# Optimization experiments

Hardware: AMD Instinct MI355X
Metric: run time of the kernel (lower is better)

## Reference

```python
import jax, jax.numpy as jnp
import numpy as np

N_MESH, N_GRID, N_EDGE = 2562, 16384, 49152
D, EDGE_DIM, OUT_DIM = 512, 4, 128
LN_EPS = 1e-5


def _mlp_ln(x, w1, b1, w2, b2, g, beta):
    # Linear -> ReLU -> Linear -> LayerNorm (activate_final=False, use_layer_norm=True)
    h = jax.nn.relu(x @ w1 + b1)
    h = h @ w2 + b2
    mu = jnp.mean(h, axis=-1, keepdims=True)
    var = jnp.var(h, axis=-1, keepdims=True)
    return (h - mu) * jax.lax.rsqrt(var + LN_EPS) * g + beta


def setup_inputs() -> dict:
    key = jax.random.key(0)
    ks = iter(jax.random.split(key, 40))

    def W(i, o):
        return (jax.random.normal(next(ks), (i, o), jnp.float32) / np.float32(np.sqrt(i)))

    inp = {
        "input_mesh_nodes": jax.random.normal(next(ks), (N_MESH, D), jnp.float32),
        "input_grid_nodes": jax.random.normal(next(ks), (N_GRID, D), jnp.float32),
        "input_edge_attr": jax.random.normal(next(ks), (N_EDGE, EDGE_DIM), jnp.float32),
        "edge_index": jnp.stack([
            jax.random.randint(next(ks), (N_EDGE,), 0, N_MESH, jnp.int32),  # senders (mesh)
            jax.random.randint(next(ks), (N_EDGE,), 0, N_GRID, jnp.int32),  # receivers (grid)
        ], axis=0),
        # edges_mlp: EDGE_DIM -> D -> D, LN
        "emlp_w1": W(EDGE_DIM, D), "emlp_b1": jnp.zeros((D,), jnp.float32),
        "emlp_w2": W(D, D), "emlp_b2": jnp.zeros((D,), jnp.float32),
        "emlp_g": jnp.ones((D,), jnp.float32), "emlp_beta": jnp.zeros((D,), jnp.float32),
        # gnn message MLP: 3D -> D -> D, LN   (cat(x_i, x_j, edge_attr))
        "ge_w1": W(3 * D, D), "ge_b1": jnp.zeros((D,), jnp.float32),
        "ge_w2": W(D, D), "ge_b2": jnp.zeros((D,), jnp.float32),
        "ge_g": jnp.ones((D,), jnp.float32), "ge_beta": jnp.zeros((D,), jnp.float32),
        # gnn node MLP: 2D -> D -> D, LN   (cat(receiver_x, aggr))
        "gn_w1": W(2 * D, D), "gn_b1": jnp.zeros((D,), jnp.float32),
        "gn_w2": W(D, D), "gn_b2": jnp.zeros((D,), jnp.float32),
        "gn_g": jnp.ones((D,), jnp.float32), "gn_beta": jnp.zeros((D,), jnp.float32),
        # grid_mlp_final: D -> D -> OUT_DIM, LN
        "fin_w1": W(D, D), "fin_b1": jnp.zeros((D,), jnp.float32),
        "fin_w2": W(D, OUT_DIM), "fin_b2": jnp.zeros((OUT_DIM,), jnp.float32),
        "fin_g": jnp.ones((OUT_DIM,), jnp.float32), "fin_beta": jnp.zeros((OUT_DIM,), jnp.float32),
    }
    return inp


def reference(input_mesh_nodes, input_grid_nodes, input_edge_attr, edge_index,
              emlp_w1, emlp_b1, emlp_w2, emlp_b2, emlp_g, emlp_beta,
              ge_w1, ge_b1, ge_w2, ge_b2, ge_g, ge_beta,
              gn_w1, gn_b1, gn_w2, gn_b2, gn_g, gn_beta,
              fin_w1, fin_b1, fin_w2, fin_b2, fin_g, fin_beta):
    # edge embedding MLP
    edges_emb = _mlp_ln(input_edge_attr, emlp_w1, emlp_b1, emlp_w2, emlp_b2, emlp_g, emlp_beta)
    senders, receivers = edge_index[0], edge_index[1]
    x_i = input_grid_nodes[receivers]   # receiver (grid) features gathered per edge
    x_j = input_mesh_nodes[senders]     # sender (mesh) features gathered per edge
    # per-edge message MLP on cat(x_i, x_j, edge_attr)
    msg = _mlp_ln(jnp.concatenate([x_i, x_j, edges_emb], axis=-1),
                  ge_w1, ge_b1, ge_w2, ge_b2, ge_g, ge_beta)  # [E, D]
    # scatter-add messages to receiver grid nodes (aggr='add')
    aggr = jax.ops.segment_sum(msg, receivers, num_segments=N_GRID)  # [N_GRID, D]
    # node update MLP on cat(receiver_x, aggr)
    gnn_out = _mlp_ln(jnp.concatenate([input_grid_nodes, aggr], axis=-1),
                      gn_w1, gn_b1, gn_w2, gn_b2, gn_g, gn_beta)
    latent_grid_nodes = input_grid_nodes + gnn_out  # residual
    return _mlp_ln(latent_grid_nodes, fin_w1, fin_b1, fin_w2, fin_b2, fin_g, fin_beta)
```

## Files before the change

### kernel.cpp

```cpp
#include <hip/hip_runtime.h>
#include <hip/hip_bf16.h>
#include <stdint.h>

#define LN_EPS 1e-5f

typedef __hip_bfloat16 bf16;
typedef short short8 __attribute__((ext_vector_type(8)));
typedef float f32x4 __attribute__((ext_vector_type(4)));

static __device__ __forceinline__ float bf2f(short s) {
    unsigned int u = ((unsigned int)(unsigned short)s) << 16;
    return __uint_as_float(u);
}
static __device__ __forceinline__ short f2bf(float x) {
    __hip_bfloat16 h = __float2bfloat16(x);
    return *reinterpret_cast<short*>(&h);
}

static __device__ __forceinline__ void gload16(const void* g, void* l) {
    __builtin_amdgcn_global_load_lds((const __attribute__((address_space(1))) void*)g,
                                     (__attribute__((address_space(3))) void*)l, 16, 0, 0);
}

struct TDesc { const float* src; bf16* dst; int K; int N; int kOff; const float* scale; };
struct TDescs { TDesc d[9]; };

__global__ void transpose_all_kernel(TDescs descs) {
    TDesc t = descs.d[blockIdx.z];
    int kb = blockIdx.x * 32, nb = blockIdx.y * 32;
    if (kb >= t.K || nb >= t.N) return;
    __shared__ float tile[32][33];
    int tx = threadIdx.x & 31, ty = threadIdx.x >> 5;
    for (int i = ty; i < 32; i += 8) {
        int k = kb + i, n = nb + tx;
        float v = (k < t.K && n < t.N) ? t.src[(size_t)(t.kOff + k) * t.N + n] : 0.f;
        if (t.scale && k < t.K) v *= t.scale[k];
        tile[i][tx] = v;
    }
    __syncthreads();
    for (int i = ty; i < 32; i += 8) {
        int n = nb + i, k = kb + tx;
        if (n < t.N && k < t.K)
            t.dst[(size_t)n * t.K + k] = __float2bfloat16(tile[tx][i]);
    }
}

__global__ void uv_kernel(const float* __restrict__ W, const float* __restrict__ g,
                          const float* __restrict__ be, float* __restrict__ u,
                          float* __restrict__ v) {
    int n = blockIdx.x * 256 + threadIdx.x;
    if (n >= 512) return;
    float su = 0.f, sv = 0.f;
    for (int k = 0; k < 512; k++) {
        float w = W[(size_t)(1024 + k) * 512 + n];
        su += g[k] * w;
        sv += be[k] * w;
    }
    u[n] = su;
    v[n] = sv;
}

__global__ void cvt_bf16_kernel(const float* __restrict__ src, bf16* __restrict__ dst, int n) {
    int i = blockIdx.x * 256 + threadIdx.x;
    int idx = i * 4;
    if (idx >= n) return;
    float4 v = *(const float4*)(src + idx);
    dst[idx + 0] = __float2bfloat16(v.x);
    dst[idx + 1] = __float2bfloat16(v.y);
    dst[idx + 2] = __float2bfloat16(v.z);
    dst[idx + 3] = __float2bfloat16(v.w);
}

__global__ void edge_l1_kernel(const float* __restrict__ attr, const float* __restrict__ w1,
                               const float* __restrict__ b1, bf16* __restrict__ h1, int E) {
    int e = blockIdx.x * 4 + (threadIdx.x >> 6);
    if (e >= E) return;
    int lane = threadIdx.x & 63;
    int d0 = lane * 8;
    float4 a = *(const float4*)(attr + (size_t)e * 4);
    float av[4] = {a.x, a.y, a.z, a.w};
    float s[8];
    {
        float4 c0 = *(const float4*)(b1 + d0), c1 = *(const float4*)(b1 + d0 + 4);
        s[0]=c0.x; s[1]=c0.y; s[2]=c0.z; s[3]=c0.w; s[4]=c1.x; s[5]=c1.y; s[6]=c1.z; s[7]=c1.w;
    }
#pragma unroll
    for (int k = 0; k < 4; k++) {
        float4 w0 = *(const float4*)(w1 + k * 512 + d0);
        float4 w1v = *(const float4*)(w1 + k * 512 + d0 + 4);
        float wv[8] = {w0.x, w0.y, w0.z, w0.w, w1v.x, w1v.y, w1v.z, w1v.w};
#pragma unroll
        for (int j = 0; j < 8; j++) s[j] += av[k] * wv[j];
    }
    short8 o;
#pragma unroll
    for (int j = 0; j < 8; j++) o[j] = f2bf(fmaxf(s[j], 0.f));
    *(short8*)(h1 + (size_t)e * 512 + d0) = o;
}

template <int EPI>
__global__ __launch_bounds__(256, 2) void gemm_bt_kernel(
    const bf16* __restrict__ A, const bf16* __restrict__ BT,
    const float* __restrict__ bias, bf16* __restrict__ C, int M, int N, int K,
    const bf16* __restrict__ gridp, const bf16* __restrict__ meshp,
    const int* __restrict__ send, const int* __restrict__ recv,
    const float2* __restrict__ stats, const float* __restrict__ uvec,
    const float* __restrict__ vvec, float* __restrict__ OutF) {
    __shared__ short SMEM[2 * 2 * 128 * 64];
    const int t = threadIdx.x;
    const int lane = t & 63, w = t >> 6;
    const int wm = w >> 1, wn = w & 1;
    const int lr = lane & 15, lh = lane >> 4;

    int gx = gridDim.x;
    int nwg = gx * gridDim.y;
    int orig = blockIdx.y * gx + blockIdx.x;
    int q = nwg >> 3, r = nwg & 7;
    int xcd = orig & 7, loc = orig >> 3;
    int wg = (xcd < r ? xcd * (q + 1) : r * (q + 1) + (xcd - r) * q) + loc;
    int bx = wg % gx, by = wg / gx;
    const int row0 = by * 128;
    const int col0 = bx * 128;

    const int sr3 = lane >> 3;
    const int su = (lane & 7) ^ sr3;
    const int srow = w * 32 + sr3;
    const int scol = su * 8;
    const bf16* gaP[4];
    const bf16* gbP[4];
#pragma unroll
    for (int i = 0; i < 4; i++) {
        int ra = row0 + srow + i * 8; if (ra >= M) ra = M - 1;
        int rb = col0 + srow + i * 8; if (rb >= N) rb = N - 1;
        gaP[i] = A + (size_t)ra * K + scol;
        gbP[i] = BT + (size_t)rb * K + scol;
    }

    auto STAGE = [&](int b, int k0) {
        short* la = SMEM + b * 16384 + w * 32 * 64;
        short* lb = la + 8192;
#pragma unroll
        for (int i = 0; i < 4; i++) {
            gload16(gaP[i] + k0, la + i * 8 * 64);
            gload16(gbP[i] + k0, lb + i * 8 * 64);
        }
    };

    f32x4 acc[4][4];
#pragma unroll
    for (int i = 0; i < 4; i++)
#pragma unroll
        for (int j = 0; j < 4; j++) acc[i][j] = {0.f, 0.f, 0.f, 0.f};

    const int T = K >> 6;
    STAGE(0, 0);

    int cur = 0;
    for (int tt = 0; tt < T; ++tt) {
        if (tt + 1 < T) {
            STAGE(cur ^ 1, (tt + 1) << 6);
            asm volatile("s_waitcnt vmcnt(8)" ::: "memory");
        } else {
            asm volatile("s_waitcnt vmcnt(0)" ::: "memory");
        }
        __builtin_amdgcn_s_barrier();
        asm volatile("" ::: "memory");

        const short* Ac = SMEM + cur * 16384;
        const short* Bc = Ac + 8192;
#pragma unroll
        for (int kk = 0; kk < 64; kk += 32) {
            short8 af[4], bfv[4];
#pragma unroll
            for (int mf = 0; mf < 4; mf++) {
                int rowa = wm * 64 + mf * 16 + lr;
                int ua = ((kk >> 3) + lh) ^ (rowa & 7);
                af[mf] = *(const short8*)&Ac[rowa * 64 + ua * 8];
            }
#pragma unroll
            for (int nf = 0; nf < 4; nf++) {
                int rowb = wn * 64 + nf * 16 + lr;
                int ub = ((kk >> 3) + lh) ^ (rowb & 7);
                bfv[nf] = *(const short8*)&Bc[rowb * 64 + ub * 8];
            }
#pragma unroll
            for (int mf = 0; mf < 4; mf++)
#pragma unroll
                for (int nf = 0; nf < 4; nf++)
                    acc[mf][nf] = __builtin_amdgcn_mfma_f32_16x16x32_bf16(
                        af[mf], bfv[nf], acc[mf][nf], 0, 0, 0);
        }
        asm volatile("" ::: "memory");
        __builtin_amdgcn_s_barrier();
        cur ^= 1;
    }

    if (EPI == 5) {
        short* Cs = SMEM;
#pragma unroll
        for (int nf = 0; nf < 4; nf++) {
            float bv = bias[wn * 64 + nf * 16 + lr];
#pragma unroll
            for (int mf = 0; mf < 4; mf++)
#pragma unroll
                for (int r2 = 0; r2 < 4; r2++) {
                    int rl = wm * 64 + mf * 16 + lh * 4 + r2;
                    Cs[rl * 132 + wn * 64 + nf * 16 + lr] = f2bf(acc[mf][nf][r2] + bv);
                }
        }
        __syncthreads();
        int rl = w * 32 + (lane >> 1);
        int half = lane & 1;
        short8 vs[8];
        float s = 0.f, s2 = 0.f;
#pragma unroll
        for (int j8 = 0; j8 < 8; j8++) {
            vs[j8] = *(const short8*)&Cs[rl * 132 + half * 64 + j8 * 8];
#pragma unroll
            for (int j = 0; j < 8; j++) {
                float f = bf2f(vs[j8][j]);
                s += f; s2 += f * f;
            }
        }
        s += __shfl_xor(s, 1, 64);
        s2 += __shfl_xor(s2, 1, 64);
        float mu = s * (1.f / 128.f);
        float var = s2 * (1.f / 128.f) - mu * mu;
        float rs = rsqrtf(var + LN_EPS);
        int grow = row0 + rl;
#pragma unroll
        for (int j8 = 0; j8 < 8; j8++) {
            int c0 = half * 64 + j8 * 8;
            float4 g0 = *(const float4*)(uvec + c0), g1 = *(const float4*)(uvec + c0 + 4);
            float4 b0 = *(const float4*)(vvec + c0), b1v = *(const float4*)(vvec + c0 + 4);
            float gg[8] = {g0.x, g0.y, g0.z, g0.w, g1.x, g1.y, g1.z, g1.w};
            float bb[8] = {b0.x, b0.y, b0.z, b0.w, b1v.x, b1v.y, b1v.z, b1v.w};
            float4 o0, o1;
            float* op = (float*)&o0;
#pragma unroll
            for (int j = 0; j < 8; j++) {
                float y = (bf2f(vs[j8][j]) - mu) * rs * gg[j] + bb[j];
                if (j < 4) ((float*)&o0)[j] = y; else ((float*)&o1)[j - 4] = y;
            }
            (void)op;
            *(float4*)(OutF + (size_t)grow * 128 + c0) = o0;
            *(float4*)(OutF + (size_t)grow * 128 + c0 + 4) = o1;
        }
        return;
    }

    short* Cw = SMEM + w * (32 * 66);
    const int rgrp = lane >> 3, u = lane & 7;
#pragma unroll
    for (int hp = 0; hp < 2; hp++) {
#pragma unroll
        for (int mf2 = 0; mf2 < 2; mf2++) {
            int mf = hp * 2 + mf2;
#pragma unroll
            for (int nf = 0; nf < 4; nf++)
#pragma unroll
                for (int r2 = 0; r2 < 4; r2++) {
                    int rl = mf2 * 16 + lh * 4 + r2;
                    Cw[rl * 66 + nf * 16 + lr] = f2bf(acc[mf][nf][r2]);
                }
        }
#pragma unroll
        for (int rr = 0; rr < 4; rr++) {
            int rl = rr * 8 + rgrp;
            int grow = row0 + wm * 64 + hp * 32 + rl;
            int gcol = col0 + wn * 64 + u * 8;
            short8 vv = *(const short8*)&Cw[rl * 66 + u * 8];
            float vf[8];
#pragma unroll
            for (int j = 0; j < 8; j++) vf[j] = bf2f(vv[j]);
            if (EPI == 4) {
                int e = grow < M ? grow : M - 1;
                float2 st = stats[e];
                float rs = st.y, mrs = st.x * st.y;
                float4 u0 = *(const float4*)(uvec + gcol), u1 = *(const float4*)(uvec + gcol + 4);
                float4 v0 = *(const float4*)(vvec + gcol), v1 = *(const float4*)(vvec + gcol + 4);
                float uu[8] = {u0.x, u0.y, u0.z, u0.w, u1.x, u1.y, u1.z, u1.w};
                float vvv[8] = {v0.x, v0.y, v0.z, v0.w, v1.x, v1.y, v1.z, v1.w};
#pragma unroll
                for (int j = 0; j < 8; j++) vf[j] = rs * vf[j] - mrs * uu[j] + vvv[j];
            }
            if (EPI >= 1) {
                float4 c0 = *(const float4*)(bias + gcol);
                float4 c1 = *(const float4*)(bias + gcol + 4);
                float bb[8] = {c0.x, c0.y, c0.z, c0.w, c1.x, c1.y, c1.z, c1.w};
#pragma unroll
                for (int j = 0; j < 8; j++) vf[j] += bb[j];
            }
            if (EPI == 4) {
                int e = grow < M ? grow : M - 1;
                int rn = recv[e], sn = send[e];
                short8 gp = *(const short8*)(gridp + (size_t)rn * 512 + gcol);
                short8 mp = *(const short8*)(meshp + (size_t)sn * 512 + gcol);
#pragma unroll
                for (int j = 0; j < 8; j++) vf[j] += bf2f(gp[j]) + bf2f(mp[j]);
            }
            if (EPI == 2 || EPI == 4) {
#pragma unroll
                for (int j = 0; j < 8; j++) vf[j] = fmaxf(vf[j], 0.f);
            }
            short8 o;
#pragma unroll
            for (int j = 0; j < 8; j++) o[j] = f2bf(vf[j]);
            if (grow < M && gcol < N)
                *(short8*)(C + (size_t)grow * N + gcol) = o;
        }
    }
}

__global__ void ln_resid_kernel(const bf16* __restrict__ X, const float* __restrict__ gw,
                                const float* __restrict__ bw, bf16* __restrict__ outb,
                                const bf16* __restrict__ resid, int R) {
    int row = blockIdx.x * 4 + (threadIdx.x >> 6);
    if (row >= R) return;
    int lane = threadIdx.x & 63;
    short8 t8 = *(const short8*)(X + (size_t)row * 512 + lane * 8);
    float v[8];
#pragma unroll
    for (int j = 0; j < 8; j++) v[j] = bf2f(t8[j]);
    float s = 0.f, s2 = 0.f;
#pragma unroll
    for (int j = 0; j < 8; j++) { s += v[j]; s2 += v[j] * v[j]; }
#pragma unroll
    for (int o = 32; o > 0; o >>= 1) {
        s += __shfl_xor(s, o, 64);
        s2 += __shfl_xor(s2, o, 64);
    }
    float mu = s * (1.f / 512.f);
    float var = s2 * (1.f / 512.f) - mu * mu;
    float rs = rsqrtf(var + LN_EPS);
    int d0 = lane * 8;
    short8 rv = *(const short8*)(resid + (size_t)row * 512 + d0);
    short8 o;
#pragma unroll
    for (int j = 0; j < 8; j++) {
        float y = (v[j] - mu) * rs * gw[d0 + j] + bw[d0 + j];
        o[j] = f2bf(bf2f(rv[j]) + y);
    }
    *(short8*)(outb + (size_t)row * 512 + d0) = o;
}

__global__ void ln_stats_kernel(const bf16* __restrict__ X, float2* __restrict__ stats, int R) {
    int row = blockIdx.x * 4 + (threadIdx.x >> 6);
    if (row >= R) return;
    int lane = threadIdx.x & 63;
    short8 t8 = *(const short8*)(X + (size_t)row * 512 + lane * 8);
    float s = 0.f, s2 = 0.f;
#pragma unroll
    for (int j = 0; j < 8; j++) {
        float x = bf2f(t8[j]);
        s += x; s2 += x * x;
    }
#pragma unroll
    for (int o = 32; o > 0; o >>= 1) {
        s += __shfl_xor(s, o, 64);
        s2 += __shfl_xor(s2, o, 64);
    }
    float mu = s * (1.f / 512.f);
    float var = s2 * (1.f / 512.f) - mu * mu;
    if (lane == 0) stats[row] = make_float2(mu, rsqrtf(var + LN_EPS));
}

__global__ void degree_kernel(const int* __restrict__ recv, int* __restrict__ deg, int E) {
    int e = blockIdx.x * 256 + threadIdx.x;
    if (e < E) atomicAdd(&deg[recv[e]], 1);
}

__global__ void scan_kernel(const int* __restrict__ deg, int* __restrict__ off) {
    __shared__ int partial[1024];
    int t = threadIdx.x;
    int base = t * 16;
    int v[16];
    int s = 0;
#pragma unroll
    for (int i = 0; i < 16; i++) { v[i] = deg[base + i]; s += v[i]; }
    partial[t] = s;
    __syncthreads();
    for (int o = 1; o < 1024; o <<= 1) {
        int x = (t >= o) ? partial[t - o] : 0;
        __syncthreads();
        partial[t] += x;
        __syncthreads();
    }
    int run = (t == 0) ? 0 : partial[t - 1];
#pragma unroll
    for (int i = 0; i < 16; i++) { off[base + i] = run; run += v[i]; }
    if (t == 1023) off[16384] = run;
}

__global__ void scatter_kernel(const int* __restrict__ recv, const int* __restrict__ off,
                               int* __restrict__ cnt, int* __restrict__ edges, int E) {
    int e = blockIdx.x * 256 + threadIdx.x;
    if (e < E) {
        int r = recv[e];
        int p = atomicAdd(&cnt[r], 1);
        edges[off[r] + p] = e;
    }
}

__global__ void aggregate_kernel(const bf16* __restrict__ T5, const float2* __restrict__ stats,
                                 const float* __restrict__ gw, const float* __restrict__ bw,
                                 const bf16* __restrict__ gridb,
                                 const int* __restrict__ off, const int* __restrict__ edges,
                                 bf16* __restrict__ X2, int G) {
    int g = blockIdx.x * 4 + (threadIdx.x >> 6);
    if (g >= G) return;
    int lane = threadIdx.x & 63;
    int d0 = lane * 8;
    float gg[8], bb[8];
    {
        float4 a = *(const float4*)(gw + d0), b = *(const float4*)(gw + d0 + 4);
        gg[0]=a.x; gg[1]=a.y; gg[2]=a.z; gg[3]=a.w; gg[4]=b.x; gg[5]=b.y; gg[6]=b.z; gg[7]=b.w;
        float4 c = *(const float4*)(bw + d0), d = *(const float4*)(bw + d0 + 4);
        bb[0]=c.x; bb[1]=c.y; bb[2]=c.z; bb[3]=c.w; bb[4]=d.x; bb[5]=d.y; bb[6]=d.z; bb[7]=d.w;
    }
    float s[8] = {0.f, 0.f, 0.f, 0.f, 0.f, 0.f, 0.f, 0.f};
    int a = off[g], b = off[g + 1];
    for (int i = a; i < b; i++) {
        int e = edges[i];
        float2 st = stats[e];
        short8 m = *(const short8*)(T5 + (size_t)e * 512 + d0);
#pragma unroll
        for (int j = 0; j < 8; j++)
            s[j] += (bf2f(m[j]) - st.x) * st.y * gg[j] + bb[j];
    }
    *(short8*)(X2 + (size_t)g * 1024 + d0) = *(const short8*)(gridb + (size_t)g * 512 + d0);
    short8 o;
#pragma unroll
    for (int j = 0; j < 8; j++) o[j] = f2bf(s[j]);
    *(short8*)(X2 + (size_t)g * 1024 + 512 + d0) = o;
}

extern "C" void kernel_launch(void* const* d_in, const int* in_sizes, int n_in,
                              void* d_out, int out_size, void* d_ws, size_t ws_size,
                              hipStream_t stream) {
    const int NM = 2562, NG = 16384, NE = 49152;
    const float* mesh   = (const float*)d_in[0];
    const float* grid   = (const float*)d_in[1];
    const float* attr   = (const float*)d_in[2];
    const int*   eidx   = (const int*)d_in[3];
    const int*   send   = eidx;
    const int*   recv   = eidx + NE;
    const float* emlp_w1 = (const float*)d_in[4];
    const float* emlp_b1 = (const float*)d_in[5];
    const float* emlp_w2 = (const float*)d_in[6];
    const float* emlp_b2 = (const float*)d_in[7];
    const float* emlp_g  = (const float*)d_in[8];
    const float* emlp_be = (const float*)d_in[9];
    const float* ge_w1 = (const float*)d_in[10];
    const float* ge_b1 = (const float*)d_in[11];
    const float* ge_w2 = (const float*)d_in[12];
    const float* ge_b2 = (const float*)d_in[13];
    const float* ge_g  = (const float*)d_in[14];
    const float* ge_be = (const float*)d_in[15];
    const float* gn_w1 = (const float*)d_in[16];
    const float* gn_b1 = (const float*)d_in[17];
    const float* gn_w2 = (const float*)d_in[18];
    const float* gn_b2 = (const float*)d_in[19];
    const float* gn_g  = (const float*)d_in[20];
    const float* gn_be = (const float*)d_in[21];
    const float* fin_w1 = (const float*)d_in[22];
    const float* fin_b1 = (const float*)d_in[23];
    const float* fin_w2 = (const float*)d_in[24];
    const float* fin_b2 = (const float*)d_in[25];
    const float* fin_g  = (const float*)d_in[26];
    const float* fin_be = (const float*)d_in[27];

    char* p = (char*)d_ws;
    auto take = [&](size_t bytes) -> char* {
        char* r = p;
        p += (bytes + 255) & ~(size_t)255;
        return r;
    };
    bf16* emlp_w2T = (bf16*)take((size_t)512 * 512 * 2);
    bf16* geA_T    = (bf16*)take((size_t)512 * 512 * 2);
    bf16* geB_T    = (bf16*)take((size_t)512 * 512 * 2);
    bf16* geC_T    = (bf16*)take((size_t)512 * 512 * 2);
    bf16* ge_w2T   = (bf16*)take((size_t)512 * 512 * 2);
    bf16* gn_w1T   = (bf16*)take((size_t)512 * 1024 * 2);
    bf16* gn_w2T   = (bf16*)take((size_t)512 * 512 * 2);
    bf16* fin_w1T  = (bf16*)take((size_t)512 * 512 * 2);
    bf16* fin_w2T  = (bf16*)take((size_t)128 * 512 * 2);
    bf16* grid_bf  = (bf16*)take((size_t)NG * 512 * 2);
    bf16* mesh_bf  = (bf16*)take((size_t)NM * 512 * 2);
    bf16* bufA     = (bf16*)take((size_t)NE * 512 * 2);
    bf16* bufB     = (bf16*)take((size_t)NE * 512 * 2);
    bf16* bufC     = (bf16*)take((size_t)NG * 512 * 2);
    bf16* bufD     = (bf16*)take((size_t)NM * 512 * 2);
    float2* stats  = (float2*)take((size_t)NE * 8);
    float* uvecW   = (float*)take((size_t)512 * 4);
    float* vvecW   = (float*)take((size_t)512 * 4);
    int*  deg      = (int*)take((size_t)NG * 4);
    int*  cnt      = (int*)take((size_t)NG * 4);
    int*  csr_off  = (int*)take((size_t)(NG + 1) * 4);
    int*  csr_edge = (int*)take((size_t)NE * 4);

    const bf16* nbf = nullptr; const int* ni = nullptr;
    const float2* nst = nullptr; const float* nf = nullptr; float* nff = nullptr;

    TDescs td;
    td.d[0] = {emlp_w2, emlp_w2T, 512, 512, 0, nullptr};
    td.d[1] = {ge_w1,   geA_T,    512, 512, 0, nullptr};
    td.d[2] = {ge_w1,   geB_T,    512, 512, 512, nullptr};
    td.d[3] = {ge_w1,   geC_T,    512, 512, 1024, emlp_g};
    td.d[4] = {ge_w2,   ge_w2T,   512, 512, 0, nullptr};
    td.d[5] = {gn_w1,   gn_w1T,  1024, 512, 0, nullptr};
    td.d[6] = {gn_w2,   gn_w2T,   512, 512, 0, nullptr};
    td.d[7] = {fin_w1,  fin_w1T,  512, 512, 0, nullptr};
    td.d[8] = {fin_w2,  fin_w2T,  512, 128, 0, nullptr};
    hipLaunchKernelGGL(transpose_all_kernel, dim3(32, 16, 9), dim3(256), 0, stream, td);
    hipLaunchKernelGGL(uv_kernel, dim3(2), dim3(256), 0, stream,
                       ge_w1, emlp_g, emlp_be, uvecW, vvecW);

    hipLaunchKernelGGL(cvt_bf16_kernel, dim3((NG * 512 / 4 + 255) / 256), dim3(256), 0, stream,
                       grid, grid_bf, NG * 512);
    hipLaunchKernelGGL(cvt_bf16_kernel, dim3((NM * 512 / 4 + 255) / 256), dim3(256), 0, stream,
                       mesh, mesh_bf, NM * 512);
    hipMemsetAsync(deg, 0, (size_t)NG * 4, stream);
    hipMemsetAsync(cnt, 0, (size_t)NG * 4, stream);
    hipLaunchKernelGGL(degree_kernel, dim3((NE + 255) / 256), dim3(256), 0, stream, recv, deg, NE);
    hipLaunchKernelGGL(scan_kernel, dim3(1), dim3(1024), 0, stream, deg, csr_off);
    hipLaunchKernelGGL(scatter_kernel, dim3((NE + 255) / 256), dim3(256), 0, stream,
                       recv, csr_off, cnt, csr_edge, NE);

    hipLaunchKernelGGL(edge_l1_kernel, dim3(NE / 4), dim3(256), 0, stream,
                       attr, emlp_w1, emlp_b1, bufA, NE);
    hipLaunchKernelGGL(gemm_bt_kernel<1>, dim3(4, NE / 128), dim3(256), 0, stream,
                       bufA, emlp_w2T, emlp_b2, bufB, NE, 512, 512,
                       nbf, nbf, ni, ni, nst, nf, nf, nff);
    hipLaunchKernelGGL(ln_stats_kernel, dim3(NE / 4), dim3(256), 0, stream, bufB, stats, NE);

    hipLaunchKernelGGL(gemm_bt_kernel<0>, dim3(4, NG / 128), dim3(256), 0, stream,
                       grid_bf, geA_T, nf, bufC, NG, 512, 512,
                       nbf, nbf, ni, ni, nst, nf, nf, nff);
    hipLaunchKernelGGL(gemm_bt_kernel<0>, dim3(4, (NM + 127) / 128), dim3(256), 0, stream,
                       mesh_bf, geB_T, nf, bufD, NM, 512, 512,
                       nbf, nbf, ni, ni, nst, nf, nf, nff);
    hipLaunchKernelGGL(gemm_bt_kernel<4>, dim3(4, NE / 128), dim3(256), 0, stream,
                       bufB, geC_T, ge_b1, bufA, NE, 512, 512,
                       bufC, bufD, send, recv, stats, uvecW, vvecW, nff);
    hipLaunchKernelGGL(gemm_bt_kernel<1>, dim3(4, NE / 128), dim3(256), 0, stream,
                       bufA, ge_w2T, ge_b2, bufB, NE, 512, 512,
                       nbf, nbf, ni, ni, nst, nf, nf, nff);
    hipLaunchKernelGGL(ln_stats_kernel, dim3(NE / 4), dim3(256), 0, stream, bufB, stats, NE);
    hipLaunchKernelGGL(aggregate_kernel, dim3(NG / 4), dim3(256), 0, stream,
                       bufB, stats, ge_g, ge_be, grid_bf, csr_off, csr_edge, bufA, NG);

    hipLaunchKernelGGL(gemm_bt_kernel<2>, dim3(4, NG / 128), dim3(256), 0, stream,
                       bufA, gn_w1T, gn_b1, bufC, NG, 512, 1024,
                       nbf, nbf, ni, ni, nst, nf, nf, nff);
    hipLaunchKernelGGL(gemm_bt_kernel<1>, dim3(4, NG / 128), dim3(256), 0, stream,
                       bufC, gn_w2T, gn_b2, bufB, NG, 512, 512,
                       nbf, nbf, ni, ni, nst, nf, nf, nff);
    hipLaunchKernelGGL(ln_resid_kernel, dim3(NG / 4), dim3(256), 0, stream,
                       bufB, gn_g, gn_be, bufA, grid_bf, NG);

    hipLaunchKernelGGL(gemm_bt_kernel<2>, dim3(4, NG / 128), dim3(256), 0, stream,
                       bufA, fin_w1T, fin_b1, bufC, NG, 512, 512,
                       nbf, nbf, ni, ni, nst, nf, nf, nff);
    hipLaunchKernelGGL(gemm_bt_kernel<5>, dim3(1, NG / 128), dim3(256), 0, stream,
                       bufC, fin_w2T, fin_b2, (bf16*)nullptr, NG, 128, 512,
                       nbf, nbf, ni, ni, nst, fin_g, fin_be, (float*)d_out);
}
```

Measured before the change: 353.2 us.

## Add 8-wave 256x128 GEMM kernel with split-K staging for large GEMMs

Adds a gemm8 kernel that uses 512 threads and a 256x128 output tile. It interleaves the A-tile prefetch with the first half-K MFMA block and the B-tile prefetch with the second half, and raises wave priority around the MFMAs. The large edge and grid GEMMs now use it, while the mesh GEMM and the final LN GEMM keep the old kernel, which is reduced to its EPI 0/5 paths. The goal is to cut B reloads per output and overlap loads with compute, at the cost of one block per CU and fewer workgroups.

```diff
diff --git a/kernel.cpp b/kernel.cpp
--- a/kernel.cpp
+++ b/kernel.cpp
@@ -99,13 +99,206 @@
 }
 
 template <int EPI>
-__global__ __launch_bounds__(256, 2) void gemm_bt_kernel(
+__global__ __launch_bounds__(512, 1) void gemm8_kernel(
     const bf16* __restrict__ A, const bf16* __restrict__ BT,
     const float* __restrict__ bias, bf16* __restrict__ C, int M, int N, int K,
     const bf16* __restrict__ gridp, const bf16* __restrict__ meshp,
     const int* __restrict__ send, const int* __restrict__ recv,
     const float2* __restrict__ stats, const float* __restrict__ uvec,
-    const float* __restrict__ vvec, float* __restrict__ OutF) {
+    const float* __restrict__ vvec) {
+    __shared__ short SMEM[2 * (256 + 128) * 64];
+    const int t = threadIdx.x;
+    const int lane = t & 63, w = t >> 6;
+    const int wm = w >> 1, wn = w & 1;
+    const int lr = lane & 15, lh = lane >> 4;
+
+    int gx = gridDim.x;
+    int nwg = gx * gridDim.y;
+    int orig = blockIdx.y * gx + blockIdx.x;
+    int q = nwg >> 3, r = nwg & 7;
+    int xcd = orig & 7, loc = orig >> 3;
+    int wg = (xcd < r ? xcd * (q + 1) : r * (q + 1) + (xcd - r) * q) + loc;
+    int bx = wg % gx, by = wg / gx;
+    const int row0 = by * 256;
+    const int col0 = bx * 128;
+
+    const int sr3 = lane >> 3;
+    const int su = (lane & 7) ^ sr3;
+    const int scol = su * 8;
+    const bf16* gaP[4];
+    const bf16* gbP[2];
+#pragma unroll
+    for (int c = 0; c < 4; c++) {
+        int ra = row0 + c * 64 + w * 8 + sr3; if (ra >= M) ra = M - 1;
+        gaP[c] = A + (size_t)ra * K + scol;
+    }
+#pragma unroll
+    for (int c = 0; c < 2; c++) {
+        int rb = col0 + c * 64 + w * 8 + sr3; if (rb >= N) rb = N - 1;
+        gbP[c] = BT + (size_t)rb * K + scol;
+    }
+
+    auto STAGE_A = [&](int b, int k0) {
+        short* la = SMEM + b * 24576;
+#pragma unroll
+        for (int c = 0; c < 4; c++)
+            gload16(gaP[c] + k0, la + (c * 64 + w * 8) * 64);
+    };
+    auto STAGE_B = [&](int b, int k0) {
+        short* lb = SMEM + b * 24576 + 16384;
+#pragma unroll
+        for (int c = 0; c < 2; c++)
+            gload16(gbP[c] + k0, lb + (c * 64 + w * 8) * 64);
+    };
+
+    f32x4 acc[4][4];
+#pragma unroll
+    for (int i = 0; i < 4; i++)
+#pragma unroll
+        for (int j = 0; j < 4; j++) acc[i][j] = {0.f, 0.f, 0.f, 0.f};
+
+    const int T = K >> 6;
+    STAGE_A(0, 0);
+    STAGE_B(0, 0);
+
+    for (int tt = 0; tt < T; ++tt) {
+        const int bc = tt & 1;
+        const int kn = (tt + 1) << 6;
+        if (tt + 1 < T) {
+            STAGE_A(bc ^ 1, kn);
+            asm volatile("s_waitcnt vmcnt(4)" ::: "memory");
+        } else {
+            asm volatile("s_waitcnt vmcnt(0)" ::: "memory");
+        }
+        __builtin_amdgcn_s_barrier();
+
+        const short* Ac = SMEM + bc * 24576;
+        const short* Bc = Ac + 16384;
+
+        {
+            short8 af[4], bfv[4];
+#pragma unroll
+            for (int mf = 0; mf < 4; mf++) {
+                int rowa = wm * 64 + mf * 16 + lr;
+                int ua = lh ^ (rowa & 7);
+                af[mf] = *(const short8*)&Ac[rowa * 64 + ua * 8];
+            }
+#pragma unroll
+            for (int nf = 0; nf < 4; nf++) {
+                int rowb = wn * 64 + nf * 16 + lr;
+                int ub = lh ^ (rowb & 7);
+                bfv[nf] = *(const short8*)&Bc[rowb * 64 + ub * 8];
+            }
+            asm volatile("" ::: "memory");
+            __builtin_amdgcn_s_barrier();
+            __builtin_amdgcn_s_setprio(1);
+#pragma unroll
+            for (int mf = 0; mf < 4; mf++)
+#pragma unroll
+                for (int nf = 0; nf < 4; nf++)
+                    acc[mf][nf] = __builtin_amdgcn_mfma_f32_16x16x32_bf16(
+                        af[mf], bfv[nf], acc[mf][nf], 0, 0, 0);
+            __builtin_amdgcn_s_setprio(0);
+        }
+        if (tt + 1 < T) STAGE_B(bc ^ 1, kn);
+        {
+            short8 af[4], bfv[4];
+#pragma unroll
+            for (int mf = 0; mf < 4; mf++) {
+                int rowa = wm * 64 + mf * 16 + lr;
+                int ua = (4 + lh) ^ (rowa & 7);
+                af[mf] = *(const short8*)&Ac[rowa * 64 + ua * 8];
+            }
+#pragma unroll
+            for (int nf = 0; nf < 4; nf++) {
+                int rowb = wn * 64 + nf * 16 + lr;
+                int ub = (4 + lh) ^ (rowb & 7);
+                bfv[nf] = *(const short8*)&Bc[rowb * 64 + ub * 8];
+            }
+            asm volatile("" ::: "memory");
+            __builtin_amdgcn_s_barrier();
+            __builtin_amdgcn_s_setprio(1);
+#pragma unroll
+            for (int mf = 0; mf < 4; mf++)
+#pragma unroll
+                for (int nf = 0; nf < 4; nf++)
+                    acc[mf][nf] = __builtin_amdgcn_mfma_f32_16x16x32_bf16(
+                        af[mf], bfv[nf], acc[mf][nf], 0, 0, 0);
+            __builtin_amdgcn_s_setprio(0);
+        }
+        asm volatile("" ::: "memory");
+        __builtin_amdgcn_s_barrier();
+    }
+
+    short* Cw = SMEM + w * (32 * 66);
+    const int rgrp = lane >> 3, u = lane & 7;
+#pragma unroll
+    for (int hp = 0; hp < 2; hp++) {
+#pragma unroll
+        for (int mf2 = 0; mf2 < 2; mf2++) {
+            int mf = hp * 2 + mf2;
+#pragma unroll
+            for (int nf = 0; nf < 4; nf++)
+#pragma unroll
+                for (int r2 = 0; r2 < 4; r2++) {
+                    int rl = mf2 * 16 + lh * 4 + r2;
+                    Cw[rl * 66 + nf * 16 + lr] = f2bf(acc[mf][nf][r2]);
+                }
+        }
+#pragma unroll
+        for (int rr = 0; rr < 4; rr++) {
+            int rl = rr * 8 + rgrp;
+            int grow = row0 + wm * 64 + hp * 32 + rl;
+            int gcol = col0 + wn * 64 + u * 8;
+            short8 vv = *(const short8*)&Cw[rl * 66 + u * 8];
+            float vf[8];
+#pragma unroll
+            for (int j = 0; j < 8; j++) vf[j] = bf2f(vv[j]);
+            if (EPI == 4) {
+                int e = grow < M ? grow : M - 1;
+                float2 st = stats[e];
+                float rs = st.y, mrs = st.x * st.y;
+                float4 u0 = *(const float4*)(uvec + gcol), u1 = *(const float4*)(uvec + gcol + 4);
+                float4 v0 = *(const float4*)(vvec + gcol), v1 = *(const float4*)(vvec + gcol + 4);
+                float uu[8] = {u0.x, u0.y, u0.z, u0.w, u1.x, u1.y, u1.z, u1.w};
+                float vvv[8] = {v0.x, v0.y, v0.z, v0.w, v1.x, v1.y, v1.z, v1.w};
+#pragma unroll
+                for (int j = 0; j < 8; j++) vf[j] = rs * vf[j] - mrs * uu[j] + vvv[j];
+            }
+            if (EPI >= 1) {
+                float4 c0 = *(const float4*)(bias + gcol);
+                float4 c1 = *(const float4*)(bias + gcol + 4);
+                float bb[8] = {c0.x, c0.y, c0.z, c0.w, c1.x, c1.y, c1.z, c1.w};
+#pragma unroll
+                for (int j = 0; j < 8; j++) vf[j] += bb[j];
+            }
+            if (EPI == 4) {
+                int e = grow < M ? grow : M - 1;
+                int rn = recv[e], sn = send[e];
+                short8 gp = *(const short8*)(gridp + (size_t)rn * 512 + gcol);
+                short8 mp = *(const short8*)(meshp + (size_t)sn * 512 + gcol);
+#pragma unroll
+                for (int j = 0; j < 8; j++) vf[j] += bf2f(gp[j]) + bf2f(mp[j]);
+            }
+            if (EPI == 2 || EPI == 4) {
+#pragma unroll
+                for (int j = 0; j < 8; j++) vf[j] = fmaxf(vf[j], 0.f);
+            }
+            short8 o;
+#pragma unroll
+            for (int j = 0; j < 8; j++) o[j] = f2bf(vf[j]);
+            if (grow < M && gcol < N)
+                *(short8*)(C + (size_t)grow * N + gcol) = o;
+        }
+    }
+}
+
+template <int EPI>
+__global__ __launch_bounds__(256, 2) void gemm_bt_kernel(
+    const bf16* __restrict__ A, const bf16* __restrict__ BT,
+    const float* __restrict__ bias, bf16* __restrict__ C, int M, int N, int K,
+    const float* __restrict__ fg, const float* __restrict__ fb,
+    float* __restrict__ OutF) {
     __shared__ short SMEM[2 * 2 * 128 * 64];
     const int t = threadIdx.x;
     const int lane = t & 63, w = t >> 6;
@@ -231,18 +424,16 @@
 #pragma unroll
         for (int j8 = 0; j8 < 8; j8++) {
             int c0 = half * 64 + j8 * 8;
-            float4 g0 = *(const float4*)(uvec + c0), g1 = *(const float4*)(uvec + c0 + 4);
-            float4 b0 = *(const float4*)(vvec + c0), b1v = *(const float4*)(vvec + c0 + 4);
+            float4 g0 = *(const float4*)(fg + c0), g1 = *(const float4*)(fg + c0 + 4);
+            float4 b0 = *(const float4*)(fb + c0), b1v = *(const float4*)(fb + c0 + 4);
             float gg[8] = {g0.x, g0.y, g0.z, g0.w, g1.x, g1.y, g1.z, g1.w};
             float bb[8] = {b0.x, b0.y, b0.z, b0.w, b1v.x, b1v.y, b1v.z, b1v.w};
             float4 o0, o1;
-            float* op = (float*)&o0;
 #pragma unroll
             for (int j = 0; j < 8; j++) {
                 float y = (bf2f(vs[j8][j]) - mu) * rs * gg[j] + bb[j];
                 if (j < 4) ((float*)&o0)[j] = y; else ((float*)&o1)[j - 4] = y;
             }
-            (void)op;
             *(float4*)(OutF + (size_t)grow * 128 + c0) = o0;
             *(float4*)(OutF + (size_t)grow * 128 + c0 + 4) = o1;
         }
@@ -270,44 +461,8 @@
             int grow = row0 + wm * 64 + hp * 32 + rl;
             int gcol = col0 + wn * 64 + u * 8;
             short8 vv = *(const short8*)&Cw[rl * 66 + u * 8];
-            float vf[8];
-#pragma unroll
-            for (int j = 0; j < 8; j++) vf[j] = bf2f(vv[j]);
-            if (EPI == 4) {
-                int e = grow < M ? grow : M - 1;
-                float2 st = stats[e];
-                float rs = st.y, mrs = st.x * st.y;
-                float4 u0 = *(const float4*)(uvec + gcol), u1 = *(const float4*)(uvec + gcol + 4);
-                float4 v0 = *(const float4*)(vvec + gcol), v1 = *(const float4*)(vvec + gcol + 4);
-                float uu[8] = {u0.x, u0.y, u0.z, u0.w, u1.x, u1.y, u1.z, u1.w};
-                float vvv[8] = {v0.x, v0.y, v0.z, v0.w, v1.x, v1.y, v1.z, v1.w};
-#pragma unroll
-                for (int j = 0; j < 8; j++) vf[j] = rs * vf[j] - mrs * uu[j] + vvv[j];
-            }
-            if (EPI >= 1) {
-                float4 c0 = *(const float4*)(bias + gcol);
-                float4 c1 = *(const float4*)(bias + gcol + 4);
-                float bb[8] = {c0.x, c0.y, c0.z, c0.w, c1.x, c1.y, c1.z, c1.w};
-#pragma unroll
-                for (int j = 0; j < 8; j++) vf[j] += bb[j];
-            }
-            if (EPI == 4) {
-                int e = grow < M ? grow : M - 1;
-                int rn = recv[e], sn = send[e];
-                short8 gp = *(const short8*)(gridp + (size_t)rn * 512 + gcol);
-                short8 mp = *(const short8*)(meshp + (size_t)sn * 512 + gcol);
-#pragma unroll
-                for (int j = 0; j < 8; j++) vf[j] += bf2f(gp[j]) + bf2f(mp[j]);
-            }
-            if (EPI == 2 || EPI == 4) {
-#pragma unroll
-                for (int j = 0; j < 8; j++) vf[j] = fmaxf(vf[j], 0.f);
-            }
-            short8 o;
-#pragma unroll
-            for (int j = 0; j < 8; j++) o[j] = f2bf(vf[j]);
             if (grow < M && gcol < N)
-                *(short8*)(C + (size_t)grow * N + gcol) = o;
+                *(short8*)(C + (size_t)grow * N + gcol) = vv;
         }
     }
 }
@@ -500,7 +655,7 @@
     int*  csr_edge = (int*)take((size_t)NE * 4);
 
     const bf16* nbf = nullptr; const int* ni = nullptr;
-    const float2* nst = nullptr; const float* nf = nullptr; float* nff = nullptr;
+    const float2* nst = nullptr; const float* nf = nullptr;
 
     TDescs td;
     td.d[0] = {emlp_w2, emlp_w2T, 512, 512, 0, nullptr};
@@ -529,40 +684,39 @@
 
     hipLaunchKernelGGL(edge_l1_kernel, dim3(NE / 4), dim3(256), 0, stream,
                        attr, emlp_w1, emlp_b1, bufA, NE);
-    hipLaunchKernelGGL(gemm_bt_kernel<1>, dim3(4, NE / 128), dim3(256), 0, stream,
+    hipLaunchKernelGGL(gemm8_kernel<1>, dim3(4, NE / 256), dim3(512), 0, stream,
                        bufA, emlp_w2T, emlp_b2, bufB, NE, 512, 512,
-                       nbf, nbf, ni, ni, nst, nf, nf, nff);
+                       nbf, nbf, ni, ni, nst, nf, nf);
     hipLaunchKernelGGL(ln_stats_kernel, dim3(NE / 4), dim3(256), 0, stream, bufB, stats, NE);
 
-    hipLaunchKernelGGL(gemm_bt_kernel<0>, dim3(4, NG / 128), dim3(256), 0, stream,
+    hipLaunchKernelGGL(gemm8_kernel<0>, dim3(4, NG / 256), dim3(512), 0, stream,
                        grid_bf, geA_T, nf, bufC, NG, 512, 512,
-                       nbf, nbf, ni, ni, nst, nf, nf, nff);
+                       nbf, nbf, ni, ni, nst, nf, nf);
     hipLaunchKernelGGL(gemm_bt_kernel<0>, dim3(4, (NM + 127) / 128), dim3(256), 0, stream,
-                       mesh_bf, geB_T, nf, bufD, NM, 512, 512,
-                       nbf, nbf, ni, ni, nst, nf, nf, nff);
-    hipLaunchKernelGGL(gemm_bt_kernel<4>, dim3(4, NE / 128), dim3(256), 0, stream,
+                       mesh_bf, geB_T, nf, bufD, NM, 512, 512, nf, nf, (float*)nullptr);
+    hipLaunchKernelGGL(gemm8_kernel<4>, dim3(4, NE / 256), dim3(512), 0, stream,
                        bufB, geC_T, ge_b1, bufA, NE, 512, 512,
-                       bufC, bufD, send, recv, stats, uvecW, vvecW, nff);
-    hipLaunchKernelGGL(gemm_bt_kernel<1>, dim3(4, NE / 128), dim3(256), 0, stream,
+                       bufC, bufD, send, recv, stats, uvecW, vvecW);
+    hipLaunchKernelGGL(gemm8_kernel<1>, dim3(4, NE / 256), dim3(512), 0, stream,
                        bufA, ge_w2T, ge_b2, bufB, NE, 512, 512,
-                       nbf, nbf, ni, ni, nst, nf, nf, nff);
+                       nbf, nbf, ni, ni, nst, nf, nf);
     hipLaunchKernelGGL(ln_stats_kernel, dim3(NE / 4), dim3(256), 0, stream, bufB, stats, NE);
     hipLaunchKernelGGL(aggregate_kernel, dim3(NG / 4), dim3(256), 0, stream,
                        bufB, stats, ge_g, ge_be, grid_bf, csr_off, csr_edge, bufA, NG);
 
-    hipLaunchKernelGGL(gemm_bt_kernel<2>, dim3(4, NG / 128), dim3(256), 0, stream,
+    hipLaunchKernelGGL(gemm8_kernel<2>, dim3(4, NG / 256), dim3(512), 0, stream,
                        bufA, gn_w1T, gn_b1, bufC, NG, 512, 1024,
-                       nbf, nbf, ni, ni, nst, nf, nf, nff);
-    hipLaunchKernelGGL(gemm_bt_kernel<1>, dim3(4, NG / 128), dim3(256), 0, stream,
+                       nbf, nbf, ni, ni, nst, nf, nf);
+    hipLaunchKernelGGL(gemm8_kernel<1>, dim3(4, NG / 256), dim3(512), 0, stream,
                        bufC, gn_w2T, gn_b2, bufB, NG, 512, 512,
-                       nbf, nbf, ni, ni, nst, nf, nf, nff);
+                       nbf, nbf, ni, ni, nst, nf, nf);
     hipLaunchKernelGGL(ln_resid_kernel, dim3(NG / 4), dim3(256), 0, stream,
                        bufB, gn_g, gn_be, bufA, grid_bf, NG);
 
-    hipLaunchKernelGGL(gemm_bt_kernel<2>, dim3(4, NG / 128), dim3(256), 0, stream,
+    hipLaunchKernelGGL(gemm8_kernel<2>, dim3(4, NG / 256), dim3(512), 0, stream,
                        bufA, fin_w1T, fin_b1, bufC, NG, 512, 512,
-                       nbf, nbf, ni, ni, nst, nf, nf, nff);
+                       nbf, nbf, ni, ni, nst, nf, nf);
     hipLaunchKernelGGL(gemm_bt_kernel<5>, dim3(1, NG / 128), dim3(256), 0, stream,
                        bufC, fin_w2T, fin_b2, (bf16*)nullptr, NG, 128, 512,
-                       nbf, nbf, ni, ni, nst, fin_g, fin_be, (float*)d_out);
-}
+                       fin_g, fin_be, (float*)d_out);
+}
```

Result: no change. 359.6 us (+1.8%).
